# Performance work log

Hardware: AMD Instinct MI355X
Metric: run time of the kernel (lower is better)

## Reference

```python
import jax, jax.numpy as jnp
import numpy as np

N_NODES = 100000
N_EDGES = 1600000
NUM_FEATS = 128
HIDDEN = 16
NUM_CLASSES = 40


def setup_inputs() -> dict:
    key = jax.random.key(0)
    k1, k2, k3, k4, k5 = jax.random.split(key, 5)
    x = jax.random.normal(k1, (N_NODES, NUM_FEATS), dtype=jnp.float32)
    edge_weight = jax.random.uniform(k2, (N_EDGES,), dtype=jnp.float32)
    # Glorot-uniform linear weights (bias=False in the module)
    lim1 = float(np.sqrt(6.0 / (NUM_FEATS + HIDDEN)))
    lim2 = float(np.sqrt(6.0 / (HIDDEN + NUM_CLASSES)))
    W1 = jax.random.uniform(k3, (NUM_FEATS, HIDDEN), dtype=jnp.float32, minval=-lim1, maxval=lim1)
    W2 = jax.random.uniform(k4, (HIDDEN, NUM_CLASSES), dtype=jnp.float32, minval=-lim2, maxval=lim2)
    edge_index = jax.random.randint(k5, (2, N_EDGES), 0, N_NODES, dtype=jnp.int64)
    return {"x": x, "edge_weight": edge_weight, "W1": W1, "W2": W2, "edge_index": edge_index}


def _sgconv(h, W, src, dst, edge_weight, n):
    # SGConv (K=1): weighted neighbor aggregation + self loop (weight 1), then bias-free linear
    msg = edge_weight[:, None] * h[src]                      # [E, d] gather + scale
    agg = jax.ops.segment_sum(msg, dst, num_segments=n) + h  # scatter-add + self loop
    return agg @ W


def reference(x, edge_weight, W1, W2, edge_index):
    src, dst = edge_index[0], edge_index[1]
    n = x.shape[0]
    h = _sgconv(x, W1, src, dst, edge_weight, n)   # [N, 16]
    # dropout(p=0.5) is identity in eval mode
    h = _sgconv(h, W2, src, dst, edge_weight, n)   # [N, num_classes]
    return jax.nn.log_softmax(h, axis=1)
```

## Files before the change

### kernel.cpp

```cpp
#include <hip/hip_runtime.h>

#define NFEAT 128
#define HID 16
#define NCLS 40
#define BSHIFT 7
#define BNODES 128
#define CAP 2560
#define NBUCK_MAX 800
#define BIN_CHUNK 4096

#define SCALE1 262144.0f
#define SCALE2 65536.0f

__device__ __forceinline__ unsigned bf16_rne(float f) {
    unsigned u = __float_as_uint(f);
    return (u + 0x7FFFu + ((u >> 16) & 1u)) >> 16;
}
__device__ __forceinline__ float bf_lo(unsigned u) { return __uint_as_float(u << 16); }
__device__ __forceinline__ float bf_hi(unsigned u) { return __uint_as_float(u & 0xFFFF0000u); }


__global__ __launch_bounds__(256) void fused_bin_gemm1_kernel(
        const int* __restrict__ src, const int* __restrict__ dst,
        const float* __restrict__ ew, int* __restrict__ cursor,
        int2* __restrict__ slab, int E, int nbuck, int nbin,
        const float* __restrict__ x, const float* __restrict__ W1,
        unsigned short* __restrict__ h1b, int n)
{
    __shared__ float smem[80 * 132];
    int tid = threadIdx.x;

    if (blockIdx.x < (unsigned)nbin) {
        int* hist    = (int*)smem;
        int* runbase = hist + NBUCK_MAX;
        for (int i = tid; i < NBUCK_MAX; i += 256) hist[i] = 0;
        __syncthreads();

        int base = blockIdx.x * BIN_CHUNK;
        int myd[16], mys[16], myw[16];
        #pragma unroll
        for (int k = 0; k < 16; ++k) {
            int e = base + k * 256 + tid;
            if (e < E) {
                myd[k] = dst[e];
                mys[k] = src[e];
                myw[k] = __float_as_int(ew[e]);
                atomicAdd(&hist[myd[k] >> BSHIFT], 1);
            } else myd[k] = -1;
        }
        __syncthreads();
        for (int i = tid; i < nbuck; i += 256) {
            int c = hist[i];
            runbase[i] = c ? (i * CAP + atomicAdd(&cursor[i], c)) : 0;
            hist[i] = 0;
        }
        __syncthreads();
        #pragma unroll
        for (int k = 0; k < 16; ++k) {
            int d = myd[k];
            if (d >= 0) {
                int b = d >> BSHIFT;
                int pos = runbase[b] + atomicAdd(&hist[b], 1);
                if (pos < (b + 1) * CAP)
                    slab[pos] = make_int2(mys[k] | ((d & (BNODES - 1)) << 20), myw[k]);
            }
        }
    } else {
        float* xs = smem;
        float* ws = smem + 64 * 132;
        int r0 = (blockIdx.x - nbin) * 64;
        int rows = n - r0; if (rows > 64) rows = 64;

        const float4* xg = (const float4*)(x + (size_t)r0 * NFEAT);
        #pragma unroll
        for (int i = 0; i < 8; ++i) {
            int flat4 = i * 256 + tid;
            int row = flat4 >> 5, k4 = flat4 & 31;
            float4 v = make_float4(0.f, 0.f, 0.f, 0.f);
            if (row < rows) v = xg[flat4];
            *(float4*)&xs[row * 132 + k4 * 4] = v;
        }
        for (int i = tid; i < HID * NFEAT; i += 256) {
            int c = i >> 7, k = i & 127;
            ws[c * 132 + k] = W1[k * HID + c];
        }
        __syncthreads();

        int row = tid >> 2;
        int c0  = (tid & 3) * 4;
        float acc[4] = {0.f, 0.f, 0.f, 0.f};
        #pragma unroll 4
        for (int k4 = 0; k4 < 32; ++k4) {
            float4 xv = *(const float4*)&xs[row * 132 + k4 * 4];
            #pragma unroll
            for (int i = 0; i < 4; ++i) {
                float4 wv = *(const float4*)&ws[(c0 + i) * 132 + k4 * 4];
                acc[i] += xv.x * wv.x + xv.y * wv.y + xv.z * wv.z + xv.w * wv.w;
            }
        }
        if (row < rows) {
            unsigned lo = bf16_rne(acc[0]) | (bf16_rne(acc[1]) << 16);
            unsigned hi = bf16_rne(acc[2]) | (bf16_rne(acc[3]) << 16);
            *(uint2*)(h1b + (size_t)(r0 + row) * HID + c0) = make_uint2(lo, hi);
        }
    }
}

__global__ __launch_bounds__(512) void gather1_kernel(const uint4* __restrict__ hq,
                                                      const int* __restrict__ cursor,
                                                      const int2* __restrict__ slab,
                                                      uint4* __restrict__ outb, int n)
{
    __shared__ int accum[HID * BNODES];
    int tid = threadIdx.x;
    #pragma unroll
    for (int i = tid; i < HID * BNODES; i += 512) accum[i] = 0;
    __syncthreads();

    int b = blockIdx.x;
    int beg = b * CAP;
    int cnt = cursor[b]; if (cnt > CAP) cnt = CAP;

    int tasks = cnt * 2;
    for (int i = tid; i < tasks; i += 512) {
        int2 e = slab[beg + (i >> 1)];
        int p = i & 1;
        int s  = e.x & 0xFFFFF;
        int dl = (e.x >> 20) & (BNODES - 1);
        float wsc = __int_as_float(e.y) * SCALE1;
        uint4 q = hq[(size_t)s * 2 + p];
        int* a = &accum[(p * 8) * BNODES + dl];
        atomicAdd(a + 0 * BNODES, __float2int_rn(wsc * bf_lo(q.x)));
        atomicAdd(a + 1 * BNODES, __float2int_rn(wsc * bf_hi(q.x)));
        atomicAdd(a + 2 * BNODES, __float2int_rn(wsc * bf_lo(q.y)));
        atomicAdd(a + 3 * BNODES, __float2int_rn(wsc * bf_hi(q.y)));
        atomicAdd(a + 4 * BNODES, __float2int_rn(wsc * bf_lo(q.z)));
        atomicAdd(a + 5 * BNODES, __float2int_rn(wsc * bf_hi(q.z)));
        atomicAdd(a + 6 * BNODES, __float2int_rn(wsc * bf_lo(q.w)));
        atomicAdd(a + 7 * BNODES, __float2int_rn(wsc * bf_hi(q.w)));
    }
    __syncthreads();

    const float inv = 1.0f / SCALE1;
    if (tid < BNODES * 2) {
        int dl = tid >> 1, p = tid & 1;
        int node = (b << BSHIFT) + dl;
        if (node < n) {
            uint4 qs = hq[(size_t)node * 2 + p];
            const int* a = &accum[(p * 8) * BNODES + dl];
            uint4 o;
            o.x = bf16_rne((float)a[0 * BNODES] * inv + bf_lo(qs.x)) |
                  (bf16_rne((float)a[1 * BNODES] * inv + bf_hi(qs.x)) << 16);
            o.y = bf16_rne((float)a[2 * BNODES] * inv + bf_lo(qs.y)) |
                  (bf16_rne((float)a[3 * BNODES] * inv + bf_hi(qs.y)) << 16);
            o.z = bf16_rne((float)a[4 * BNODES] * inv + bf_lo(qs.z)) |
                  (bf16_rne((float)a[5 * BNODES] * inv + bf_hi(qs.z)) << 16);
            o.w = bf16_rne((float)a[6 * BNODES] * inv + bf_lo(qs.w)) |
                  (bf16_rne((float)a[7 * BNODES] * inv + bf_hi(qs.w)) << 16);
            outb[(size_t)node * 2 + p] = o;
        }
    }
}

#define ZPAD 41
__global__ __launch_bounds__(512) void gather2_lsm_kernel(const uint4* __restrict__ hq,
                                                          const int* __restrict__ cursor,
                                                          const int2* __restrict__ slab,
                                                          const float* __restrict__ W2,
                                                          float* __restrict__ out, int n)
{
    __shared__ int   accum[HID * BNODES];
    __shared__ float w2s[HID * NCLS];
    __shared__ float zbuf[BNODES * ZPAD];
    int tid = threadIdx.x;
    #pragma unroll
    for (int i = tid; i < HID * BNODES; i += 512) accum[i] = 0;
    for (int i = tid; i < HID * NCLS; i += 512) w2s[i] = W2[i];
    __syncthreads();

    int b = blockIdx.x;
    int beg = b * CAP;
    int cnt = cursor[b]; if (cnt > CAP) cnt = CAP;
    int node0 = b << BSHIFT;

    int tasks = cnt * 2;
    for (int i = tid; i < tasks; i += 512) {
        int2 e = slab[beg + (i >> 1)];
        int p = i & 1;
        int s  = e.x & 0xFFFFF;
        int dl = (e.x >> 20) & (BNODES - 1);
        float wsc = __int_as_float(e.y) * SCALE2;
        uint4 q = hq[(size_t)s * 2 + p];
        int* a = &accum[(p * 8) * BNODES + dl];
        atomicAdd(a + 0 * BNODES, __float2int_rn(wsc * bf_lo(q.x)));
        atomicAdd(a + 1 * BNODES, __float2int_rn(wsc * bf_hi(q.x)));
        atomicAdd(a + 2 * BNODES, __float2int_rn(wsc * bf_lo(q.y)));
        atomicAdd(a + 3 * BNODES, __float2int_rn(wsc * bf_hi(q.y)));
        atomicAdd(a + 4 * BNODES, __float2int_rn(wsc * bf_lo(q.z)));
        atomicAdd(a + 5 * BNODES, __float2int_rn(wsc * bf_hi(q.z)));
        atomicAdd(a + 6 * BNODES, __float2int_rn(wsc * bf_lo(q.w)));
        atomicAdd(a + 7 * BNODES, __float2int_rn(wsc * bf_hi(q.w)));
    }
    __syncthreads();

    const float inv = 1.0f / SCALE2;
    if (tid < BNODES) {
        int dl = tid;
        int node = node0 + dl;
        if (node < n) {
            uint4 q0 = hq[(size_t)node * 2 + 0];
            uint4 q1 = hq[(size_t)node * 2 + 1];
            float r[HID];
            r[0]  = (float)accum[ 0 * BNODES + dl] * inv + bf_lo(q0.x);
            r[1]  = (float)accum[ 1 * BNODES + dl] * inv + bf_hi(q0.x);
            r[2]  = (float)accum[ 2 * BNODES + dl] * inv + bf_lo(q0.y);
            r[3]  = (float)accum[ 3 * BNODES + dl] * inv + bf_hi(q0.y);
            r[4]  = (float)accum[ 4 * BNODES + dl] * inv + bf_lo(q0.z);
            r[5]  = (float)accum[ 5 * BNODES + dl] * inv + bf_hi(q0.z);
            r[6]  = (float)accum[ 6 * BNODES + dl] * inv + bf_lo(q0.w);
            r[7]  = (float)accum[ 7 * BNODES + dl] * inv + bf_hi(q0.w);
            r[8]  = (float)accum[ 8 * BNODES + dl] * inv + bf_lo(q1.x);
            r[9]  = (float)accum[ 9 * BNODES + dl] * inv + bf_hi(q1.x);
            r[10] = (float)accum[10 * BNODES + dl] * inv + bf_lo(q1.y);
            r[11] = (float)accum[11 * BNODES + dl] * inv + bf_hi(q1.y);
            r[12] = (float)accum[12 * BNODES + dl] * inv + bf_lo(q1.z);
            r[13] = (float)accum[13 * BNODES + dl] * inv + bf_hi(q1.z);
            r[14] = (float)accum[14 * BNODES + dl] * inv + bf_lo(q1.w);
            r[15] = (float)accum[15 * BNODES + dl] * inv + bf_hi(q1.w);

            float z[NCLS];
            #pragma unroll
            for (int j = 0; j < NCLS; ++j) z[j] = 0.f;
            #pragma unroll
            for (int f = 0; f < HID; ++f) {
                float rf = r[f];
                #pragma unroll
                for (int j = 0; j < NCLS; ++j)
                    z[j] += rf * w2s[f * NCLS + j];
            }
            float m = z[0];
            #pragma unroll
            for (int j = 1; j < NCLS; ++j) m = fmaxf(m, z[j]);
            float ssum = 0.f;
            #pragma unroll
            for (int j = 0; j < NCLS; ++j) ssum += __expf(z[j] - m);
            float l = m + __logf(ssum);
            #pragma unroll
            for (int j = 0; j < NCLS; ++j) zbuf[dl * ZPAD + j] = z[j] - l;
        }
    }
    __syncthreads();

    for (int i = tid; i < BNODES * NCLS; i += 512) {
        int nl = i / NCLS, j = i - nl * NCLS;
        if (node0 + nl < n)
            out[(size_t)node0 * NCLS + i] = zbuf[nl * ZPAD + j];
    }
}

extern "C" void kernel_launch(void* const* d_in, const int* in_sizes, int n_in,
                              void* d_out, int out_size, void* d_ws, size_t ws_size,
                              hipStream_t stream)
{
    const float* x  = (const float*)d_in[0];
    const float* ew = (const float*)d_in[1];
    const float* W1 = (const float*)d_in[2];
    const float* W2 = (const float*)d_in[3];
    const int*   ei = (const int*)d_in[4];

    int n = in_sizes[0] / NFEAT;
    int E = in_sizes[1];
    const int* src = ei;
    const int* dst = ei + E;
    float* out = (float*)d_out;

    int nbuck = (n + BNODES - 1) >> BSHIFT;
    int nbin  = (E + BIN_CHUNK - 1) / BIN_CHUNK;
    int ngemm = (n + 63) / 64;

    char* w = (char*)d_ws;
    int*  cursor = (int*)w;  w += NBUCK_MAX * 4;
    w = (char*)(((size_t)w + 15) & ~(size_t)15);
    int2* slab   = (int2*)w; w += (size_t)NBUCK_MAX * CAP * 8;
    unsigned short* h1b = (unsigned short*)w; w += (size_t)n * HID * 2;
    unsigned short* h2b = (unsigned short*)w; w += (size_t)n * HID * 2;

    hipMemsetAsync(cursor, 0, (size_t)nbuck * 4, stream);
    fused_bin_gemm1_kernel<<<nbin + ngemm, 256, 0, stream>>>(
        src, dst, ew, cursor, slab, E, nbuck, nbin, x, W1, h1b, n);
    gather1_kernel<<<nbuck, 512, 0, stream>>>((const uint4*)h1b, cursor, slab,
                                              (uint4*)h2b, n);
    gather2_lsm_kernel<<<nbuck, 512, 0, stream>>>((const uint4*)h2b, cursor, slab,
                                                  W2, out, n);
}
```

Measured before the change: 186.0 us.

## Split bin/GEMM kernels, use bf16 MFMA for GEMM1, pipeline gathers, pad accum layout

The fused bin+GEMM1 kernel is split into a standalone binning kernel and a GEMM1 kernel that uses bf16 MFMA 16x16x32 instructions, loading x directly from global memory with no LDS staging. Both gather kernels gain a software-pipelined loop that prefetches the next slab entry and the next feature row ahead of the LDS atomics. The LDS accumulator layout changes from feature-major to node-major with a padding of 17 to alter the bank pattern of the atomics. Inputs to GEMM1 are now rounded to bf16, which lowers precision, and the split adds one more kernel launch while losing the overlap the fused kernel gave.

```diff
diff --git a/kernel.cpp b/kernel.cpp
--- a/kernel.cpp
+++ b/kernel.cpp
@@ -8,9 +8,13 @@
 #define CAP 2560
 #define NBUCK_MAX 800
 #define BIN_CHUNK 4096
+#define APAD 17
 
 #define SCALE1 262144.0f
 #define SCALE2 65536.0f
+
+typedef __attribute__((ext_vector_type(8))) short short8;
+typedef __attribute__((ext_vector_type(4))) float f32x4;
 
 __device__ __forceinline__ unsigned bf16_rne(float f) {
     unsigned u = __float_as_uint(f);
@@ -19,90 +23,87 @@
 __device__ __forceinline__ float bf_lo(unsigned u) { return __uint_as_float(u << 16); }
 __device__ __forceinline__ float bf_hi(unsigned u) { return __uint_as_float(u & 0xFFFF0000u); }
 
-
-__global__ __launch_bounds__(256) void fused_bin_gemm1_kernel(
-        const int* __restrict__ src, const int* __restrict__ dst,
-        const float* __restrict__ ew, int* __restrict__ cursor,
-        int2* __restrict__ slab, int E, int nbuck, int nbin,
-        const float* __restrict__ x, const float* __restrict__ W1,
-        unsigned short* __restrict__ h1b, int n)
-{
-    __shared__ float smem[80 * 132];
+__global__ __launch_bounds__(256) void bin_kernel(const int* __restrict__ src,
+                                                  const int* __restrict__ dst,
+                                                  const float* __restrict__ ew,
+                                                  int* __restrict__ cursor,
+                                                  int2* __restrict__ slab,
+                                                  int E, int nbuck)
+{
+    __shared__ int hist[NBUCK_MAX];
+    __shared__ int runbase[NBUCK_MAX];
     int tid = threadIdx.x;
-
-    if (blockIdx.x < (unsigned)nbin) {
-        int* hist    = (int*)smem;
-        int* runbase = hist + NBUCK_MAX;
-        for (int i = tid; i < NBUCK_MAX; i += 256) hist[i] = 0;
-        __syncthreads();
-
-        int base = blockIdx.x * BIN_CHUNK;
-        int myd[16], mys[16], myw[16];
+    for (int i = tid; i < NBUCK_MAX; i += 256) hist[i] = 0;
+    __syncthreads();
+
+    int base = blockIdx.x * BIN_CHUNK;
+    int myd[16], mys[16], myw[16];
+    #pragma unroll
+    for (int k = 0; k < 16; ++k) {
+        int e = base + k * 256 + tid;
+        if (e < E) {
+            myd[k] = dst[e];
+            mys[k] = src[e];
+            myw[k] = __float_as_int(ew[e]);
+            atomicAdd(&hist[myd[k] >> BSHIFT], 1);
+        } else myd[k] = -1;
+    }
+    __syncthreads();
+    for (int i = tid; i < nbuck; i += 256) {
+        int c = hist[i];
+        runbase[i] = c ? (i * CAP + atomicAdd(&cursor[i], c)) : 0;
+        hist[i] = 0;
+    }
+    __syncthreads();
+    #pragma unroll
+    for (int k = 0; k < 16; ++k) {
+        int d = myd[k];
+        if (d >= 0) {
+            int b = d >> BSHIFT;
+            int pos = runbase[b] + atomicAdd(&hist[b], 1);
+            if (pos < (b + 1) * CAP)
+                slab[pos] = make_int2(mys[k] | ((d & (BNODES - 1)) << 20), myw[k]);
+        }
+    }
+}
+
+__global__ __launch_bounds__(256) void gemm1_mfma_kernel(const float* __restrict__ x,
+                                                         const float* __restrict__ W1,
+                                                         unsigned short* __restrict__ h1b,
+                                                         int n)
+{
+    int tid  = threadIdx.x;
+    int wave = tid >> 6, lane = tid & 63;
+    int m = lane & 15, q = lane >> 4;
+    int base = blockIdx.x * 64 + wave * 16;
+
+    short8 bfrag[4];
+    #pragma unroll
+    for (int kc = 0; kc < 4; ++kc) {
         #pragma unroll
-        for (int k = 0; k < 16; ++k) {
-            int e = base + k * 256 + tid;
-            if (e < E) {
-                myd[k] = dst[e];
-                mys[k] = src[e];
-                myw[k] = __float_as_int(ew[e]);
-                atomicAdd(&hist[myd[k] >> BSHIFT], 1);
-            } else myd[k] = -1;
-        }
-        __syncthreads();
-        for (int i = tid; i < nbuck; i += 256) {
-            int c = hist[i];
-            runbase[i] = c ? (i * CAP + atomicAdd(&cursor[i], c)) : 0;
-            hist[i] = 0;
-        }
-        __syncthreads();
-        #pragma unroll
-        for (int k = 0; k < 16; ++k) {
-            int d = myd[k];
-            if (d >= 0) {
-                int b = d >> BSHIFT;
-                int pos = runbase[b] + atomicAdd(&hist[b], 1);
-                if (pos < (b + 1) * CAP)
-                    slab[pos] = make_int2(mys[k] | ((d & (BNODES - 1)) << 20), myw[k]);
-            }
-        }
-    } else {
-        float* xs = smem;
-        float* ws = smem + 64 * 132;
-        int r0 = (blockIdx.x - nbin) * 64;
-        int rows = n - r0; if (rows > 64) rows = 64;
-
-        const float4* xg = (const float4*)(x + (size_t)r0 * NFEAT);
-        #pragma unroll
-        for (int i = 0; i < 8; ++i) {
-            int flat4 = i * 256 + tid;
-            int row = flat4 >> 5, k4 = flat4 & 31;
-            float4 v = make_float4(0.f, 0.f, 0.f, 0.f);
-            if (row < rows) v = xg[flat4];
-            *(float4*)&xs[row * 132 + k4 * 4] = v;
-        }
-        for (int i = tid; i < HID * NFEAT; i += 256) {
-            int c = i >> 7, k = i & 127;
-            ws[c * 132 + k] = W1[k * HID + c];
-        }
-        __syncthreads();
-
-        int row = tid >> 2;
-        int c0  = (tid & 3) * 4;
-        float acc[4] = {0.f, 0.f, 0.f, 0.f};
-        #pragma unroll 4
-        for (int k4 = 0; k4 < 32; ++k4) {
-            float4 xv = *(const float4*)&xs[row * 132 + k4 * 4];
-            #pragma unroll
-            for (int i = 0; i < 4; ++i) {
-                float4 wv = *(const float4*)&ws[(c0 + i) * 132 + k4 * 4];
-                acc[i] += xv.x * wv.x + xv.y * wv.y + xv.z * wv.z + xv.w * wv.w;
-            }
-        }
-        if (row < rows) {
-            unsigned lo = bf16_rne(acc[0]) | (bf16_rne(acc[1]) << 16);
-            unsigned hi = bf16_rne(acc[2]) | (bf16_rne(acc[3]) << 16);
-            *(uint2*)(h1b + (size_t)(r0 + row) * HID + c0) = make_uint2(lo, hi);
-        }
+        for (int j = 0; j < 8; ++j)
+            bfrag[kc][j] = (short)bf16_rne(W1[(kc * 32 + q * 8 + j) * HID + m]);
+    }
+
+    int rowa = base + m; if (rowa > n - 1) rowa = n - 1;
+    const float* xr = x + (size_t)rowa * NFEAT;
+    f32x4 acc = {0.f, 0.f, 0.f, 0.f};
+    #pragma unroll
+    for (int kc = 0; kc < 4; ++kc) {
+        float4 a0 = *(const float4*)(xr + kc * 32 + q * 8);
+        float4 a1 = *(const float4*)(xr + kc * 32 + q * 8 + 4);
+        short8 af;
+        af[0] = (short)bf16_rne(a0.x); af[1] = (short)bf16_rne(a0.y);
+        af[2] = (short)bf16_rne(a0.z); af[3] = (short)bf16_rne(a0.w);
+        af[4] = (short)bf16_rne(a1.x); af[5] = (short)bf16_rne(a1.y);
+        af[6] = (short)bf16_rne(a1.z); af[7] = (short)bf16_rne(a1.w);
+        acc = __builtin_amdgcn_mfma_f32_16x16x32_bf16(af, bfrag[kc], acc, 0, 0, 0);
+    }
+    #pragma unroll
+    for (int reg = 0; reg < 4; ++reg) {
+        int rowd = base + q * 4 + reg;
+        if (rowd < n)
+            h1b[(size_t)rowd * HID + m] = (unsigned short)bf16_rne(acc[reg]);
     }
 }
 
@@ -111,33 +112,44 @@
                                                       const int2* __restrict__ slab,
                                                       uint4* __restrict__ outb, int n)
 {
-    __shared__ int accum[HID * BNODES];
+    __shared__ int accum[BNODES * APAD];
     int tid = threadIdx.x;
     #pragma unroll
-    for (int i = tid; i < HID * BNODES; i += 512) accum[i] = 0;
+    for (int i = tid; i < BNODES * APAD; i += 512) accum[i] = 0;
     __syncthreads();
 
     int b = blockIdx.x;
     int beg = b * CAP;
     int cnt = cursor[b]; if (cnt > CAP) cnt = CAP;
-
-    int tasks = cnt * 2;
-    for (int i = tid; i < tasks; i += 512) {
-        int2 e = slab[beg + (i >> 1)];
-        int p = i & 1;
-        int s  = e.x & 0xFFFFF;
-        int dl = (e.x >> 20) & (BNODES - 1);
-        float wsc = __int_as_float(e.y) * SCALE1;
-        uint4 q = hq[(size_t)s * 2 + p];
-        int* a = &accum[(p * 8) * BNODES + dl];
-        atomicAdd(a + 0 * BNODES, __float2int_rn(wsc * bf_lo(q.x)));
-        atomicAdd(a + 1 * BNODES, __float2int_rn(wsc * bf_hi(q.x)));
-        atomicAdd(a + 2 * BNODES, __float2int_rn(wsc * bf_lo(q.y)));
-        atomicAdd(a + 3 * BNODES, __float2int_rn(wsc * bf_hi(q.y)));
-        atomicAdd(a + 4 * BNODES, __float2int_rn(wsc * bf_lo(q.z)));
-        atomicAdd(a + 5 * BNODES, __float2int_rn(wsc * bf_hi(q.z)));
-        atomicAdd(a + 6 * BNODES, __float2int_rn(wsc * bf_lo(q.w)));
-        atomicAdd(a + 7 * BNODES, __float2int_rn(wsc * bf_hi(q.w)));
+    int total = cnt * 2;
+
+    int i0 = tid, i1 = tid + 512;
+    int2 e0, e1; uint4 q0;
+    if (i0 < total) e0 = slab[beg + (i0 >> 1)];
+    if (i1 < total) e1 = slab[beg + (i1 >> 1)];
+    if (i0 < total) q0 = hq[(size_t)(e0.x & 0xFFFFF) * 2 + (i0 & 1)];
+
+    while (i0 < total) {
+        uint4 q1;
+        if (i1 < total) q1 = hq[(size_t)(e1.x & 0xFFFFF) * 2 + (i1 & 1)];
+        int i2 = i1 + 512;
+        int2 e2;
+        if (i2 < total) e2 = slab[beg + (i2 >> 1)];
+
+        int p  = i0 & 1;
+        int dl = (e0.x >> 20) & (BNODES - 1);
+        float wsc = __int_as_float(e0.y) * SCALE1;
+        int* a = &accum[dl * APAD + p * 8];
+        atomicAdd(a + 0, __float2int_rn(wsc * bf_lo(q0.x)));
+        atomicAdd(a + 1, __float2int_rn(wsc * bf_hi(q0.x)));
+        atomicAdd(a + 2, __float2int_rn(wsc * bf_lo(q0.y)));
+        atomicAdd(a + 3, __float2int_rn(wsc * bf_hi(q0.y)));
+        atomicAdd(a + 4, __float2int_rn(wsc * bf_lo(q0.z)));
+        atomicAdd(a + 5, __float2int_rn(wsc * bf_hi(q0.z)));
+        atomicAdd(a + 6, __float2int_rn(wsc * bf_lo(q0.w)));
+        atomicAdd(a + 7, __float2int_rn(wsc * bf_hi(q0.w)));
+
+        e0 = e1; e1 = e2; q0 = q1; i0 = i1; i1 = i2;
     }
     __syncthreads();
 
@@ -147,16 +159,16 @@
         int node = (b << BSHIFT) + dl;
         if (node < n) {
             uint4 qs = hq[(size_t)node * 2 + p];
-            const int* a = &accum[(p * 8) * BNODES + dl];
+            const int* a = &accum[dl * APAD + p * 8];
             uint4 o;
-            o.x = bf16_rne((float)a[0 * BNODES] * inv + bf_lo(qs.x)) |
-                  (bf16_rne((float)a[1 * BNODES] * inv + bf_hi(qs.x)) << 16);
-            o.y = bf16_rne((float)a[2 * BNODES] * inv + bf_lo(qs.y)) |
-                  (bf16_rne((float)a[3 * BNODES] * inv + bf_hi(qs.y)) << 16);
-            o.z = bf16_rne((float)a[4 * BNODES] * inv + bf_lo(qs.z)) |
-                  (bf16_rne((float)a[5 * BNODES] * inv + bf_hi(qs.z)) << 16);
-            o.w = bf16_rne((float)a[6 * BNODES] * inv + bf_lo(qs.w)) |
-                  (bf16_rne((float)a[7 * BNODES] * inv + bf_hi(qs.w)) << 16);
+            o.x = bf16_rne((float)a[0] * inv + bf_lo(qs.x)) |
+                  (bf16_rne((float)a[1] * inv + bf_hi(qs.x)) << 16);
+            o.y = bf16_rne((float)a[2] * inv + bf_lo(qs.y)) |
+                  (bf16_rne((float)a[3] * inv + bf_hi(qs.y)) << 16);
+            o.z = bf16_rne((float)a[4] * inv + bf_lo(qs.z)) |
+                  (bf16_rne((float)a[5] * inv + bf_hi(qs.z)) << 16);
+            o.w = bf16_rne((float)a[6] * inv + bf_lo(qs.w)) |
+                  (bf16_rne((float)a[7] * inv + bf_hi(qs.w)) << 16);
             outb[(size_t)node * 2 + p] = o;
         }
     }
@@ -169,12 +181,12 @@
                                                           const float* __restrict__ W2,
                                                           float* __restrict__ out, int n)
 {
-    __shared__ int   accum[HID * BNODES];
+    __shared__ int   accum[BNODES * APAD];
     __shared__ float w2s[HID * NCLS];
     __shared__ float zbuf[BNODES * ZPAD];
     int tid = threadIdx.x;
     #pragma unroll
-    for (int i = tid; i < HID * BNODES; i += 512) accum[i] = 0;
+    for (int i = tid; i < BNODES * APAD; i += 512) accum[i] = 0;
     for (int i = tid; i < HID * NCLS; i += 512) w2s[i] = W2[i];
     __syncthreads();
 
@@ -182,24 +194,35 @@
     int beg = b * CAP;
     int cnt = cursor[b]; if (cnt > CAP) cnt = CAP;
     int node0 = b << BSHIFT;
-
-    int tasks = cnt * 2;
-    for (int i = tid; i < tasks; i += 512) {
-        int2 e = slab[beg + (i >> 1)];
-        int p = i & 1;
-        int s  = e.x & 0xFFFFF;
-        int dl = (e.x >> 20) & (BNODES - 1);
-        float wsc = __int_as_float(e.y) * SCALE2;
-        uint4 q = hq[(size_t)s * 2 + p];
-        int* a = &accum[(p * 8) * BNODES + dl];
-        atomicAdd(a + 0 * BNODES, __float2int_rn(wsc * bf_lo(q.x)));
-        atomicAdd(a + 1 * BNODES, __float2int_rn(wsc * bf_hi(q.x)));
-        atomicAdd(a + 2 * BNODES, __float2int_rn(wsc * bf_lo(q.y)));
-        atomicAdd(a + 3 * BNODES, __float2int_rn(wsc * bf_hi(q.y)));
-        atomicAdd(a + 4 * BNODES, __float2int_rn(wsc * bf_lo(q.z)));
-        atomicAdd(a + 5 * BNODES, __float2int_rn(wsc * bf_hi(q.z)));
-        atomicAdd(a + 6 * BNODES, __float2int_rn(wsc * bf_lo(q.w)));
-        atomicAdd(a + 7 * BNODES, __float2int_rn(wsc * bf_hi(q.w)));
+    int total = cnt * 2;
+
+    int i0 = tid, i1 = tid + 512;
+    int2 e0, e1; uint4 q0;
+    if (i0 < total) e0 = slab[beg + (i0 >> 1)];
+    if (i1 < total) e1 = slab[beg + (i1 >> 1)];
+    if (i0 < total) q0 = hq[(size_t)(e0.x & 0xFFFFF) * 2 + (i0 & 1)];
+
+    while (i0 < total) {
+        uint4 q1;
+        if (i1 < total) q1 = hq[(size_t)(e1.x & 0xFFFFF) * 2 + (i1 & 1)];
+        int i2 = i1 + 512;
+        int2 e2;
+        if (i2 < total) e2 = slab[beg + (i2 >> 1)];
+
+        int p  = i0 & 1;
+        int dl = (e0.x >> 20) & (BNODES - 1);
+        float wsc = __int_as_float(e0.y) * SCALE2;
+        int* a = &accum[dl * APAD + p * 8];
+        atomicAdd(a + 0, __float2int_rn(wsc * bf_lo(q0.x)));
+        atomicAdd(a + 1, __float2int_rn(wsc * bf_hi(q0.x)));
+        atomicAdd(a + 2, __float2int_rn(wsc * bf_lo(q0.y)));
+        atomicAdd(a + 3, __float2int_rn(wsc * bf_hi(q0.y)));
+        atomicAdd(a + 4, __float2int_rn(wsc * bf_lo(q0.z)));
+        atomicAdd(a + 5, __float2int_rn(wsc * bf_hi(q0.z)));
+        atomicAdd(a + 6, __float2int_rn(wsc * bf_lo(q0.w)));
+        atomicAdd(a + 7, __float2int_rn(wsc * bf_hi(q0.w)));
+
+        e0 = e1; e1 = e2; q0 = q1; i0 = i1; i1 = i2;
     }
     __syncthreads();
 
@@ -208,25 +231,26 @@
         int dl = tid;
         int node = node0 + dl;
         if (node < n) {
-            uint4 q0 = hq[(size_t)node * 2 + 0];
-            uint4 q1 = hq[(size_t)node * 2 + 1];
+            uint4 qa = hq[(size_t)node * 2 + 0];
+            uint4 qb = hq[(size_t)node * 2 + 1];
             float r[HID];
-            r[0]  = (float)accum[ 0 * BNODES + dl] * inv + bf_lo(q0.x);
-            r[1]  = (float)accum[ 1 * BNODES + dl] * inv + bf_hi(q0.x);
-            r[2]  = (float)accum[ 2 * BNODES + dl] * inv + bf_lo(q0.y);
-            r[3]  = (float)accum[ 3 * BNODES + dl] * inv + bf_hi(q0.y);
-            r[4]  = (float)accum[ 4 * BNODES + dl] * inv + bf_lo(q0.z);
-            r[5]  = (float)accum[ 5 * BNODES + dl] * inv + bf_hi(q0.z);
-            r[6]  = (float)accum[ 6 * BNODES + dl] * inv + bf_lo(q0.w);
-            r[7]  = (float)accum[ 7 * BNODES + dl] * inv + bf_hi(q0.w);
-            r[8]  = (float)accum[ 8 * BNODES + dl] * inv + bf_lo(q1.x);
-            r[9]  = (float)accum[ 9 * BNODES + dl] * inv + bf_hi(q1.x);
-            r[10] = (float)accum[10 * BNODES + dl] * inv + bf_lo(q1.y);
-            r[11] = (float)accum[11 * BNODES + dl] * inv + bf_hi(q1.y);
-            r[12] = (float)accum[12 * BNODES + dl] * inv + bf_lo(q1.z);
-            r[13] = (float)accum[13 * BNODES + dl] * inv + bf_hi(q1.z);
-            r[14] = (float)accum[14 * BNODES + dl] * inv + bf_lo(q1.w);
-            r[15] = (float)accum[15 * BNODES + dl] * inv + bf_hi(q1.w);
+            const int* a = &accum[dl * APAD];
+            r[0]  = (float)a[ 0] * inv + bf_lo(qa.x);
+            r[1]  = (float)a[ 1] * inv + bf_hi(qa.x);
+            r[2]  = (float)a[ 2] * inv + bf_lo(qa.y);
+            r[3]  = (float)a[ 3] * inv + bf_hi(qa.y);
+            r[4]  = (float)a[ 4] * inv + bf_lo(qa.z);
+            r[5]  = (float)a[ 5] * inv + bf_hi(qa.z);
+            r[6]  = (float)a[ 6] * inv + bf_lo(qa.w);
+            r[7]  = (float)a[ 7] * inv + bf_hi(qa.w);
+            r[8]  = (float)a[ 8] * inv + bf_lo(qb.x);
+            r[9]  = (float)a[ 9] * inv + bf_hi(qb.x);
+            r[10] = (float)a[10] * inv + bf_lo(qb.y);
+            r[11] = (float)a[11] * inv + bf_hi(qb.y);
+            r[12] = (float)a[12] * inv + bf_lo(qb.z);
+            r[13] = (float)a[13] * inv + bf_hi(qb.z);
+            r[14] = (float)a[14] * inv + bf_lo(qb.w);
+            r[15] = (float)a[15] * inv + bf_hi(qb.w);
 
             float z[NCLS];
             #pragma unroll
@@ -276,7 +300,6 @@
 
     int nbuck = (n + BNODES - 1) >> BSHIFT;
     int nbin  = (E + BIN_CHUNK - 1) / BIN_CHUNK;
-    int ngemm = (n + 63) / 64;
 
     char* w = (char*)d_ws;
     int*  cursor = (int*)w;  w += NBUCK_MAX * 4;
@@ -286,8 +309,8 @@
     unsigned short* h2b = (unsigned short*)w; w += (size_t)n * HID * 2;
 
     hipMemsetAsync(cursor, 0, (size_t)nbuck * 4, stream);
-    fused_bin_gemm1_kernel<<<nbin + ngemm, 256, 0, stream>>>(
-        src, dst, ew, cursor, slab, E, nbuck, nbin, x, W1, h1b, n);
+    bin_kernel<<<nbin, 256, 0, stream>>>(src, dst, ew, cursor, slab, E, nbuck);
+    gemm1_mfma_kernel<<<(n + 63) / 64, 256, 0, stream>>>(x, W1, h1b, n);
     gather1_kernel<<<nbuck, 512, 0, stream>>>((const uint4*)h1b, cursor, slab,
                                               (uint4*)h2b, n);
     gather2_lsm_kernel<<<nbuck, 512, 0, stream>>>((const uint4*)h2b, cursor, slab,
```

Result: faster. 175.0 us (-5.9%).
